# Kernel optimization log

Measured on AMD Instinct MI355X. Metric: run time of the kernel, lower is better.

The kernel has to match this reference:

```python
import jax, jax.numpy as jnp
import numpy as np

N_NODES = 50000
N_EDGES = 800000
IN_CH, HID_CH, OUT_CH = 128, 128, 64


def setup_inputs() -> dict:
    key = jax.random.key(0)
    k1, k2, k3, k4, k5, k6 = jax.random.split(key, 6)
    x = jax.random.normal(k1, (N_NODES, IN_CH), dtype=jnp.float32)
    edge_index = jax.random.randint(k2, (2, N_EDGES), 0, N_NODES, dtype=jnp.int64)
    # nn.Linear params: W [out, in], b [out]
    W1 = jax.random.normal(k3, (HID_CH, IN_CH), dtype=jnp.float32) / np.sqrt(IN_CH)
    b1 = jax.random.normal(k4, (HID_CH,), dtype=jnp.float32) * 0.01
    W2 = jax.random.normal(k5, (OUT_CH, HID_CH), dtype=jnp.float32) / np.sqrt(HID_CH)
    b2 = jax.random.normal(k6, (OUT_CH,), dtype=jnp.float32) * 0.01
    return {"x": x, "edge_index": edge_index, "W1": W1, "b1": b1, "W2": W2, "b2": b2}


def _aggregate(x, edge_index):
    # Faithful to SimpleGNN.aggregate: deg from ROW counts, normalization gathered at DST (col).
    row, col = edge_index[0], edge_index[1]
    n = x.shape[0]
    deg = jnp.bincount(row, length=n).astype(x.dtype)
    deg_inv = jnp.where(deg > 0, 1.0 / deg, 0.0)
    # out[dst] += x[src] * deg_inv[dst]  ==  segment_sum(x[src] by dst) * deg_inv[dst]
    agg = jax.ops.segment_sum(x[row], col, num_segments=n)
    return agg * deg_inv[:, None]


def reference(x, edge_index, W1, b1, W2, b2):
    h = x @ W1.T + b1                 # [N, hidden]
    h = _aggregate(h, edge_index)     # degree-normalized scatter-add
    out = h @ W2.T + b2               # [N, out]
    return out
```

## Files before the change

kernel.cpp:

```cpp
#include <hip/hip_runtime.h>
#include <hip/hip_bf16.h>


#define IN_CH   128
#define OUT_CH  64
#define NCHUNK  128
#define LGCHUNK 7
#define NRANGE  8
#define RBINS   6272
#define MC_BLOCKS 33
#define YROWS   32

typedef unsigned short u16;
typedef unsigned int u32;

static __device__ inline float bfu32_lo(u32 u) { return __uint_as_float(u << 16); }
static __device__ inline float bfu32_hi(u32 u) { return __uint_as_float(u & 0xffff0000u); }
static __device__ inline u16 f2bf(float f) {
    __hip_bfloat16 h = __float2bfloat16(f);
    return *reinterpret_cast<u16*>(&h);
}

static __device__ inline int detect_stride_wave(const int* __restrict__ ei) {
    int lane = threadIdx.x & 63;
    int idx = (lane < 32) ? (2 * lane + 1) : 1;
    int v = ei[idx];
    unsigned long long m = __ballot((v != 0) && (lane < 32));
    return (m == 0ull) ? 2 : 1;
}

__global__ __launch_bounds__(256) void mk_prep(const float* __restrict__ W1,
                                               const float* __restrict__ b1,
                                               const float* __restrict__ W2,
                                               const int* __restrict__ ei,
                                               float* __restrict__ M,
                                               float* __restrict__ c,
                                               u16* __restrict__ row_slab,
                                               u16* __restrict__ col_slab,
                                               int n_edges, int n_nodes) {
    __shared__ u32 bins[RBINS];
    int b = blockIdx.x;
    int tid = threadIdx.x;
    if (b < MC_BLOCKS) {
        int t = b * 256 + tid;
        if (t < IN_CH * OUT_CH) {
            int o = t & (OUT_CH - 1);
            int i = t >> 6;
            float acc = 0.f;
            for (int h = 0; h < 128; ++h)
                acc += W1[h * 128 + i] * W2[o * 128 + h];
            M[i * OUT_CH + o] = acc;
        } else if (t < IN_CH * OUT_CH + OUT_CH) {
            int o = t - IN_CH * OUT_CH;
            float acc = 0.f;
            for (int h = 0; h < 128; ++h)
                acc += b1[h] * W2[o * 128 + h];
            c[o] = acc;
        }
        return;
    }
    int hb = b - MC_BLOCKS;
    int chunk = hb & (NCHUNK - 1);
    int range = hb >> LGCHUNK;

    int range_size = (n_nodes + NRANGE - 1) / NRANGE;
    int lo = range * range_size;
    int hi = lo + range_size; if (hi > n_nodes) hi = n_nodes;
    int nbins = hi - lo;
    if (nbins <= 0) return;

    int stride = detect_stride_wave(ei);
    for (int i = tid; i < nbins; i += 256) bins[i] = 0u;
    __syncthreads();

    size_t e0 = (size_t)chunk * n_edges / NCHUNK;
    size_t e1 = (size_t)(chunk + 1) * n_edges / NCHUNK;
    size_t cnt = e1 - e0;
    const int* rp = ei;
    const int* cp = ei + (size_t)n_edges * stride;

    size_t i = tid;
    int s[8], d[8];
    for (; i + 1792 < cnt; i += 2048) {
#pragma unroll
        for (int k = 0; k < 8; ++k) s[k] = rp[(e0 + i + 256 * k) * stride];
#pragma unroll
        for (int k = 0; k < 8; ++k) d[k] = cp[(e0 + i + 256 * k) * stride];
#pragma unroll
        for (int k = 0; k < 8; ++k) {
            if (s[k] >= lo && s[k] < hi) atomicAdd(&bins[s[k] - lo], 1u);
            if (d[k] >= lo && d[k] < hi && (unsigned)s[k] < (unsigned)n_nodes)
                atomicAdd(&bins[d[k] - lo], 0x10000u);
        }
    }
    for (; i < cnt; i += 256) {
        int ss = rp[(e0 + i) * stride];
        int dd = cp[(e0 + i) * stride];
        if (ss >= lo && ss < hi) atomicAdd(&bins[ss - lo], 1u);
        if (dd >= lo && dd < hi && (unsigned)ss < (unsigned)n_nodes)
            atomicAdd(&bins[dd - lo], 0x10000u);
    }
    __syncthreads();

    size_t base = (size_t)chunk * n_nodes + lo;
    for (int k = tid; k < nbins; k += 256) {
        u32 v = bins[k];
        row_slab[base + k] = (u16)(v & 0xFFFFu);
        col_slab[base + k] = (u16)(v >> 16);
    }
}

__global__ __launch_bounds__(256) void mk_y_choff(const float* __restrict__ x,
                                                  const float* __restrict__ M,
                                                  u16* __restrict__ y,
                                                  u16* __restrict__ row_slab,
                                                  u16* __restrict__ col_slab,
                                                  int* __restrict__ deg_row,
                                                  int* __restrict__ cnt_col,
                                                  int* __restrict__ cursor_part,
                                                  int* __restrict__ bsums,
                                                  int n_nodes, int y_blocks) {
    __shared__ float smem[IN_CH * OUT_CH + YROWS * (IN_CH + 4)];
    int b = blockIdx.x;
    int tid = threadIdx.x;

    if (b < y_blocks) {
        float* Ms = smem;
        float (*xs)[IN_CH + 4] = (float(*)[IN_CH + 4])(smem + IN_CH * OUT_CH);
        int tx = tid & 15;
        int ty = tid >> 4;
        int row0 = b * YROWS;

        const float4* Mv = (const float4*)M;
        float4* Msv = (float4*)Ms;
#pragma unroll
        for (int k = 0; k < 8; ++k) Msv[tid + 256 * k] = Mv[tid + 256 * k];

        for (int f = tid; f < YROWS * 32; f += 256) {
            int r = f >> 5, kq = f & 31;
            float4 v = make_float4(0.f, 0.f, 0.f, 0.f);
            if (row0 + r < n_nodes)
                v = *(const float4*)&x[(size_t)(row0 + r) * IN_CH + 4 * kq];
            *(float4*)&xs[r][4 * kq] = v;
        }
        __syncthreads();

        float4 acc0 = make_float4(0.f, 0.f, 0.f, 0.f);
        float4 acc1 = make_float4(0.f, 0.f, 0.f, 0.f);

        for (int k = 0; k < IN_CH; k += 4) {
            float4 xr0 = *(const float4*)&xs[ty][k];
            float4 xr1 = *(const float4*)&xs[ty + 16][k];
            float4 m0 = *(const float4*)&Ms[(k + 0) * OUT_CH + 4 * tx];
            float4 m1 = *(const float4*)&Ms[(k + 1) * OUT_CH + 4 * tx];
            float4 m2 = *(const float4*)&Ms[(k + 2) * OUT_CH + 4 * tx];
            float4 m3 = *(const float4*)&Ms[(k + 3) * OUT_CH + 4 * tx];
            acc0.x = fmaf(xr0.x, m0.x, acc0.x); acc0.y = fmaf(xr0.x, m0.y, acc0.y);
            acc0.z = fmaf(xr0.x, m0.z, acc0.z); acc0.w = fmaf(xr0.x, m0.w, acc0.w);
            acc0.x = fmaf(xr0.y, m1.x, acc0.x); acc0.y = fmaf(xr0.y, m1.y, acc0.y);
            acc0.z = fmaf(xr0.y, m1.z, acc0.z); acc0.w = fmaf(xr0.y, m1.w, acc0.w);
            acc0.x = fmaf(xr0.z, m2.x, acc0.x); acc0.y = fmaf(xr0.z, m2.y, acc0.y);
            acc0.z = fmaf(xr0.z, m2.z, acc0.z); acc0.w = fmaf(xr0.z, m2.w, acc0.w);
            acc0.x = fmaf(xr0.w, m3.x, acc0.x); acc0.y = fmaf(xr0.w, m3.y, acc0.y);
            acc0.z = fmaf(xr0.w, m3.z, acc0.z); acc0.w = fmaf(xr0.w, m3.w, acc0.w);
            acc1.x = fmaf(xr1.x, m0.x, acc1.x); acc1.y = fmaf(xr1.x, m0.y, acc1.y);
            acc1.z = fmaf(xr1.x, m0.z, acc1.z); acc1.w = fmaf(xr1.x, m0.w, acc1.w);
            acc1.x = fmaf(xr1.y, m1.x, acc1.x); acc1.y = fmaf(xr1.y, m1.y, acc1.y);
            acc1.z = fmaf(xr1.y, m1.z, acc1.z); acc1.w = fmaf(xr1.y, m1.w, acc1.w);
            acc1.x = fmaf(xr1.z, m2.x, acc1.x); acc1.y = fmaf(xr1.z, m2.y, acc1.y);
            acc1.z = fmaf(xr1.z, m2.z, acc1.z); acc1.w = fmaf(xr1.z, m2.w, acc1.w);
            acc1.x = fmaf(xr1.w, m3.x, acc1.x); acc1.y = fmaf(xr1.w, m3.y, acc1.y);
            acc1.z = fmaf(xr1.w, m3.z, acc1.z); acc1.w = fmaf(xr1.w, m3.w, acc1.w);
        }

        int r0 = row0 + ty;
        int r1 = row0 + ty + 16;
        if (r0 < n_nodes) {
            ushort4 s4;
            s4.x = f2bf(acc0.x); s4.y = f2bf(acc0.y);
            s4.z = f2bf(acc0.z); s4.w = f2bf(acc0.w);
            *(ushort4*)&y[(size_t)r0 * OUT_CH + 4 * tx] = s4;
        }
        if (r1 < n_nodes) {
            ushort4 s4;
            s4.x = f2bf(acc1.x); s4.y = f2bf(acc1.y);
            s4.z = f2bf(acc1.z); s4.w = f2bf(acc1.w);
            *(ushort4*)&y[(size_t)r1 * OUT_CH + 4 * tx] = s4;
        }
        return;
    }

    int* sm = (int*)smem;
    int t = tid;
    int n = (b - y_blocks) * 256 + t;
    int run = 0;
    if (n < n_nodes) {
        int sum = 0;
#pragma unroll 8
        for (int ch = 0; ch < NCHUNK; ++ch)
            sum += row_slab[(size_t)ch * n_nodes + n];
        deg_row[n] = sum;
#pragma unroll 8
        for (int ch = 0; ch < NCHUNK; ++ch) {
            int v = col_slab[(size_t)ch * n_nodes + n];
            col_slab[(size_t)ch * n_nodes + n] = (u16)run;
            run += v;
        }
        cnt_col[n] = run;
    }
    sm[t] = run;
    __syncthreads();
    for (int d = 1; d < 256; d <<= 1) {
        int add = (t >= d) ? sm[t - d] : 0;
        __syncthreads();
        sm[t] += add;
        __syncthreads();
    }
    if (n < n_nodes) cursor_part[n] = sm[t] - run;
    if (t == 255) bsums[b - y_blocks] = sm[t];
}

static __device__ void block_bscan(const int* __restrict__ bsums, int nb,
                                   int* __restrict__ bscan) {
    int t = threadIdx.x;
    int v = (t < nb) ? bsums[t] : 0;
    bscan[t] = v;
    __syncthreads();
    for (int d = 1; d < 256; d <<= 1) {
        int add = (t >= d) ? bscan[t - d] : 0;
        __syncthreads();
        bscan[t] += add;
        __syncthreads();
    }
    bscan[t] -= v;
    __syncthreads();
}

__global__ __launch_bounds__(256) void mk_place(const int* __restrict__ ei,
                                                const int* __restrict__ cursor_part,
                                                const int* __restrict__ bsums,
                                                const u16* __restrict__ col_slab,
                                                int* __restrict__ csr_src,
                                                int n_edges, int n_nodes, int nb) {
    __shared__ int rank[RBINS];
    __shared__ int bscan[256];
    block_bscan(bsums, nb, bscan);

    int b = blockIdx.x;
    int chunk = b & (NCHUNK - 1);
    int range = b >> LGCHUNK;

    int range_size = (n_nodes + NRANGE - 1) / NRANGE;
    int lo = range * range_size;
    int hi = lo + range_size; if (hi > n_nodes) hi = n_nodes;
    if (hi <= lo) return;

    int stride = detect_stride_wave(ei);
    for (int i = threadIdx.x; i < hi - lo; i += 256) rank[i] = 0;
    __syncthreads();

    size_t e0 = (size_t)chunk * n_edges / NCHUNK;
    size_t e1 = (size_t)(chunk + 1) * n_edges / NCHUNK;
    size_t cnt = e1 - e0;
    const int* rp = ei;
    const int* cp = ei + (size_t)n_edges * stride;
    size_t slab_base = (size_t)chunk * n_nodes;

    size_t i = threadIdx.x;
    int s[8], d[8], cpart[8], coff[8];
    for (; i + 1792 < cnt; i += 2048) {
#pragma unroll
        for (int k = 0; k < 8; ++k) s[k] = rp[(e0 + i + 256 * k) * stride];
#pragma unroll
        for (int k = 0; k < 8; ++k) d[k] = cp[(e0 + i + 256 * k) * stride];
#pragma unroll
        for (int k = 0; k < 8; ++k) {
            int dc = (d[k] >= lo && d[k] < hi) ? d[k] : lo;
            cpart[k] = cursor_part[dc];
            coff[k]  = (int)col_slab[slab_base + dc];
        }
#pragma unroll
        for (int k = 0; k < 8; ++k) {
            if (d[k] >= lo && d[k] < hi && (unsigned)s[k] < (unsigned)n_nodes) {
                int r = atomicAdd(&rank[d[k] - lo], 1);
                csr_src[cpart[k] + bscan[d[k] >> 8] + coff[k] + r] = s[k];
            }
        }
    }
    for (; i < cnt; i += 256) {
        int ss = rp[(e0 + i) * stride];
        int dd = cp[(e0 + i) * stride];
        if (dd >= lo && dd < hi && (unsigned)ss < (unsigned)n_nodes) {
            int r = atomicAdd(&rank[dd - lo], 1);
            csr_src[cursor_part[dd] + bscan[dd >> 8] + (int)col_slab[slab_base + dd] + r] = ss;
        }
    }
}

__global__ __launch_bounds__(256) void mk_agg_final(const int* __restrict__ cursor_part,
                                                    const int* __restrict__ bsums,
                                                    const int* __restrict__ cnt_col,
                                                    const int* __restrict__ csr_src,
                                                    const int* __restrict__ deg_row,
                                                    const uint2* __restrict__ yv,
                                                    const float* __restrict__ c,
                                                    const float* __restrict__ b2,
                                                    float* __restrict__ out,
                                                    int n_nodes, int nb) {
    __shared__ int bscan[256];
    block_bscan(bsums, nb, bscan);

    int wave = threadIdx.x >> 6;
    int lane = threadIdx.x & 63;
    int dsub = lane >> 4;
    int ch   = lane & 15;
    int d = blockIdx.x * 16 + wave * 4 + dsub;
    if (d >= n_nodes) return;

    int start = cursor_part[d] + bscan[d >> 8];
    int cnt = cnt_col[d];
    int end = start + cnt;
    int e1m = end - 1;
    float a0 = 0.f, a1 = 0.f, a2 = 0.f, a3 = 0.f;
    for (int j = start; j < end; j += 8) {
        int idx[8], srcs[8];
#pragma unroll
        for (int k = 0; k < 8; ++k) {
            int t = j + k;
            idx[k] = t > e1m ? e1m : t;
        }
#pragma unroll
        for (int k = 0; k < 8; ++k) srcs[k] = csr_src[idx[k]];
        uint2 u[8];
#pragma unroll
        for (int k = 0; k < 8; ++k) u[k] = yv[(size_t)srcs[k] * 16 + ch];
#pragma unroll
        for (int k = 1; k < 8; ++k)
            if (j + k >= end) { u[k].x = 0u; u[k].y = 0u; }
#pragma unroll
        for (int k = 0; k < 8; ++k) {
            a0 += bfu32_lo(u[k].x);
            a1 += bfu32_hi(u[k].x);
            a2 += bfu32_lo(u[k].y);
            a3 += bfu32_hi(u[k].y);
        }
    }
    int dr = deg_row[d];
    float di = (dr > 0) ? (1.0f / (float)dr) : 0.f;
    float fc = di * (float)cnt;
    float4 cv = ((const float4*)c)[ch];
    float4 bv = ((const float4*)b2)[ch];
    float4 o;
    o.x = di * a0 + fc * cv.x + bv.x;
    o.y = di * a1 + fc * cv.y + bv.y;
    o.z = di * a2 + fc * cv.z + bv.z;
    o.w = di * a3 + fc * cv.w + bv.w;
    ((float4*)(out + (size_t)d * OUT_CH))[ch] = o;
}

extern "C" void kernel_launch(void* const* d_in, const int* in_sizes, int n_in,
                              void* d_out, int out_size, void* d_ws, size_t ws_size,
                              hipStream_t stream) {
    const float* x  = (const float*)d_in[0];
    const int*   ei = (const int*)d_in[1];
    const float* W1 = (const float*)d_in[2];
    const float* b1 = (const float*)d_in[3];
    const float* W2 = (const float*)d_in[4];
    const float* b2 = (const float*)d_in[5];
    float* out = (float*)d_out;

    const int n_nodes = in_sizes[0] / IN_CH;
    const int n_edges = in_sizes[1] / 2;

    const size_t slab_bytes = (((size_t)NCHUNK * n_nodes * 2) + 127) & ~(size_t)127;
    const size_t csr_bytes  = ((size_t)n_edges * 4 + 127) & ~(size_t)127;

    char* ws = (char*)d_ws;
    float* M        = (float*)(ws);
    float* c        = (float*)(ws + 32768);
    int*   deg_row  = (int*)  (ws + 33152);
    int*   cnt_col  = (int*)  (ws + 233216);
    int*   cursor   = (int*)  (ws + 433280);
    int*   bsums    = (int*)  (ws + 633344);
    u16*   row_slab = (u16*)  (ws + 637440);
    u16*   col_slab = (u16*)  (ws + 637440 + slab_bytes);
    int*   csr_src  = (int*)  (ws + 637440 + 2 * slab_bytes);
    u16*   y        = (u16*)  (ws + 637440 + 2 * slab_bytes + csr_bytes);

    const int y_blocks = (n_nodes + YROWS - 1) / YROWS;
    const int nb = (n_nodes + 255) / 256;

    mk_prep<<<MC_BLOCKS + NCHUNK * NRANGE, 256, 0, stream>>>(
        W1, b1, W2, ei, M, c, row_slab, col_slab, n_edges, n_nodes);

    mk_y_choff<<<y_blocks + nb, 256, 0, stream>>>(
        x, M, y, row_slab, col_slab, deg_row, cnt_col, cursor, bsums,
        n_nodes, y_blocks);

    mk_place<<<NCHUNK * NRANGE, 256, 0, stream>>>(
        ei, cursor, bsums, col_slab, csr_src, n_edges, n_nodes, nb);

    mk_agg_final<<<(n_nodes + 15) / 16, 256, 0, stream>>>(
        cursor, bsums, cnt_col, csr_src, deg_row, (const uint2*)y, c, b2, out,
        n_nodes, nb);
}
```

Measured before the change: 165.9 us.

## Move y GEMM into place kernel and halve edge chunk count

The x·M projection blocks move out of the prefix-sum kernel and into the CSR placement kernel, so the scan kernel is small and the GEMM overlaps with the edge scatter. The edge histogram uses 64 chunks instead of 128, which halves the slab size and the per-node work in the scan. Blocks are reordered so range is the fast index, and the M-compute blocks are padded to 40. Fewer chunks means each histogram/place block handles more edges, so there is less parallelism in those phases.

After: 154.9 us. 1.07x faster.

```diff
diff --git a/kernel.cpp b/kernel.cpp
--- a/kernel.cpp
+++ b/kernel.cpp
@@ -4,12 +4,14 @@
 
 #define IN_CH   128
 #define OUT_CH  64
-#define NCHUNK  128
-#define LGCHUNK 7
+#define NCHUNK  64
 #define NRANGE  8
 #define RBINS   6272
 #define MC_BLOCKS 33
+#define MC_PAD  40
 #define YROWS   32
+#define PLACE_BLOCKS (NCHUNK * NRANGE)
+#define SMEM_FLOATS (IN_CH * OUT_CH + YROWS * (IN_CH + 4))
 
 typedef unsigned short u16;
 typedef unsigned int u32;
@@ -41,7 +43,7 @@
     __shared__ u32 bins[RBINS];
     int b = blockIdx.x;
     int tid = threadIdx.x;
-    if (b < MC_BLOCKS) {
+    if (b < MC_PAD) {
         int t = b * 256 + tid;
         if (t < IN_CH * OUT_CH) {
             int o = t & (OUT_CH - 1);
@@ -59,9 +61,9 @@
         }
         return;
     }
-    int hb = b - MC_BLOCKS;
-    int chunk = hb & (NCHUNK - 1);
-    int range = hb >> LGCHUNK;
+    int hb = b - MC_PAD;
+    int range = hb & (NRANGE - 1);
+    int chunk = hb >> 3;
 
     int range_size = (n_nodes + NRANGE - 1) / NRANGE;
     int lo = range * range_size;
@@ -110,89 +112,16 @@
     }
 }
 
-__global__ __launch_bounds__(256) void mk_y_choff(const float* __restrict__ x,
-                                                  const float* __restrict__ M,
-                                                  u16* __restrict__ y,
-                                                  u16* __restrict__ row_slab,
-                                                  u16* __restrict__ col_slab,
-                                                  int* __restrict__ deg_row,
-                                                  int* __restrict__ cnt_col,
-                                                  int* __restrict__ cursor_part,
-                                                  int* __restrict__ bsums,
-                                                  int n_nodes, int y_blocks) {
-    __shared__ float smem[IN_CH * OUT_CH + YROWS * (IN_CH + 4)];
-    int b = blockIdx.x;
-    int tid = threadIdx.x;
-
-    if (b < y_blocks) {
-        float* Ms = smem;
-        float (*xs)[IN_CH + 4] = (float(*)[IN_CH + 4])(smem + IN_CH * OUT_CH);
-        int tx = tid & 15;
-        int ty = tid >> 4;
-        int row0 = b * YROWS;
-
-        const float4* Mv = (const float4*)M;
-        float4* Msv = (float4*)Ms;
-#pragma unroll
-        for (int k = 0; k < 8; ++k) Msv[tid + 256 * k] = Mv[tid + 256 * k];
-
-        for (int f = tid; f < YROWS * 32; f += 256) {
-            int r = f >> 5, kq = f & 31;
-            float4 v = make_float4(0.f, 0.f, 0.f, 0.f);
-            if (row0 + r < n_nodes)
-                v = *(const float4*)&x[(size_t)(row0 + r) * IN_CH + 4 * kq];
-            *(float4*)&xs[r][4 * kq] = v;
-        }
-        __syncthreads();
-
-        float4 acc0 = make_float4(0.f, 0.f, 0.f, 0.f);
-        float4 acc1 = make_float4(0.f, 0.f, 0.f, 0.f);
-
-        for (int k = 0; k < IN_CH; k += 4) {
-            float4 xr0 = *(const float4*)&xs[ty][k];
-            float4 xr1 = *(const float4*)&xs[ty + 16][k];
-            float4 m0 = *(const float4*)&Ms[(k + 0) * OUT_CH + 4 * tx];
-            float4 m1 = *(const float4*)&Ms[(k + 1) * OUT_CH + 4 * tx];
-            float4 m2 = *(const float4*)&Ms[(k + 2) * OUT_CH + 4 * tx];
-            float4 m3 = *(const float4*)&Ms[(k + 3) * OUT_CH + 4 * tx];
-            acc0.x = fmaf(xr0.x, m0.x, acc0.x); acc0.y = fmaf(xr0.x, m0.y, acc0.y);
-            acc0.z = fmaf(xr0.x, m0.z, acc0.z); acc0.w = fmaf(xr0.x, m0.w, acc0.w);
-            acc0.x = fmaf(xr0.y, m1.x, acc0.x); acc0.y = fmaf(xr0.y, m1.y, acc0.y);
-            acc0.z = fmaf(xr0.y, m1.z, acc0.z); acc0.w = fmaf(xr0.y, m1.w, acc0.w);
-            acc0.x = fmaf(xr0.z, m2.x, acc0.x); acc0.y = fmaf(xr0.z, m2.y, acc0.y);
-            acc0.z = fmaf(xr0.z, m2.z, acc0.z); acc0.w = fmaf(xr0.z, m2.w, acc0.w);
-            acc0.x = fmaf(xr0.w, m3.x, acc0.x); acc0.y = fmaf(xr0.w, m3.y, acc0.y);
-            acc0.z = fmaf(xr0.w, m3.z, acc0.z); acc0.w = fmaf(xr0.w, m3.w, acc0.w);
-            acc1.x = fmaf(xr1.x, m0.x, acc1.x); acc1.y = fmaf(xr1.x, m0.y, acc1.y);
-            acc1.z = fmaf(xr1.x, m0.z, acc1.z); acc1.w = fmaf(xr1.x, m0.w, acc1.w);
-            acc1.x = fmaf(xr1.y, m1.x, acc1.x); acc1.y = fmaf(xr1.y, m1.y, acc1.y);
-            acc1.z = fmaf(xr1.y, m1.z, acc1.z); acc1.w = fmaf(xr1.y, m1.w, acc1.w);
-            acc1.x = fmaf(xr1.z, m2.x, acc1.x); acc1.y = fmaf(xr1.z, m2.y, acc1.y);
-            acc1.z = fmaf(xr1.z, m2.z, acc1.z); acc1.w = fmaf(xr1.z, m2.w, acc1.w);
-            acc1.x = fmaf(xr1.w, m3.x, acc1.x); acc1.y = fmaf(xr1.w, m3.y, acc1.y);
-            acc1.z = fmaf(xr1.w, m3.z, acc1.z); acc1.w = fmaf(xr1.w, m3.w, acc1.w);
-        }
-
-        int r0 = row0 + ty;
-        int r1 = row0 + ty + 16;
-        if (r0 < n_nodes) {
-            ushort4 s4;
-            s4.x = f2bf(acc0.x); s4.y = f2bf(acc0.y);
-            s4.z = f2bf(acc0.z); s4.w = f2bf(acc0.w);
-            *(ushort4*)&y[(size_t)r0 * OUT_CH + 4 * tx] = s4;
-        }
-        if (r1 < n_nodes) {
-            ushort4 s4;
-            s4.x = f2bf(acc1.x); s4.y = f2bf(acc1.y);
-            s4.z = f2bf(acc1.z); s4.w = f2bf(acc1.w);
-            *(ushort4*)&y[(size_t)r1 * OUT_CH + 4 * tx] = s4;
-        }
-        return;
-    }
-
-    int* sm = (int*)smem;
-    int t = tid;
-    int n = (b - y_blocks) * 256 + t;
+__global__ __launch_bounds__(256) void mk_choff(u16* __restrict__ row_slab,
+                                                u16* __restrict__ col_slab,
+                                                int* __restrict__ deg_row,
+                                                int* __restrict__ cnt_col,
+                                                int* __restrict__ cursor_part,
+                                                int* __restrict__ bsums,
+                                                int n_nodes) {
+    __shared__ int sm[256];
+    int t = threadIdx.x;
+    int n = blockIdx.x * 256 + t;
     int run = 0;
     if (n < n_nodes) {
         int sum = 0;
@@ -217,7 +146,7 @@
         __syncthreads();
     }
     if (n < n_nodes) cursor_part[n] = sm[t] - run;
-    if (t == 255) bsums[b - y_blocks] = sm[t];
+    if (t == 255) bsums[blockIdx.x] = sm[t];
 }
 
 static __device__ void block_bscan(const int* __restrict__ bsums, int nb,
@@ -236,64 +165,137 @@
     __syncthreads();
 }
 
-__global__ __launch_bounds__(256) void mk_place(const int* __restrict__ ei,
-                                                const int* __restrict__ cursor_part,
-                                                const int* __restrict__ bsums,
-                                                const u16* __restrict__ col_slab,
-                                                int* __restrict__ csr_src,
-                                                int n_edges, int n_nodes, int nb) {
-    __shared__ int rank[RBINS];
-    __shared__ int bscan[256];
-    block_bscan(bsums, nb, bscan);
-
+__global__ __launch_bounds__(256) void mk_place_y(const int* __restrict__ ei,
+                                                  const int* __restrict__ cursor_part,
+                                                  const int* __restrict__ bsums,
+                                                  const u16* __restrict__ col_slab,
+                                                  int* __restrict__ csr_src,
+                                                  const float* __restrict__ x,
+                                                  const float* __restrict__ M,
+                                                  u16* __restrict__ y,
+                                                  int n_edges, int n_nodes, int nb) {
+    __shared__ float smem[SMEM_FLOATS];
     int b = blockIdx.x;
-    int chunk = b & (NCHUNK - 1);
-    int range = b >> LGCHUNK;
-
-    int range_size = (n_nodes + NRANGE - 1) / NRANGE;
-    int lo = range * range_size;
-    int hi = lo + range_size; if (hi > n_nodes) hi = n_nodes;
-    if (hi <= lo) return;
-
-    int stride = detect_stride_wave(ei);
-    for (int i = threadIdx.x; i < hi - lo; i += 256) rank[i] = 0;
-    __syncthreads();
-
-    size_t e0 = (size_t)chunk * n_edges / NCHUNK;
-    size_t e1 = (size_t)(chunk + 1) * n_edges / NCHUNK;
-    size_t cnt = e1 - e0;
-    const int* rp = ei;
-    const int* cp = ei + (size_t)n_edges * stride;
-    size_t slab_base = (size_t)chunk * n_nodes;
-
-    size_t i = threadIdx.x;
-    int s[8], d[8], cpart[8], coff[8];
-    for (; i + 1792 < cnt; i += 2048) {
-#pragma unroll
-        for (int k = 0; k < 8; ++k) s[k] = rp[(e0 + i + 256 * k) * stride];
-#pragma unroll
-        for (int k = 0; k < 8; ++k) d[k] = cp[(e0 + i + 256 * k) * stride];
-#pragma unroll
-        for (int k = 0; k < 8; ++k) {
-            int dc = (d[k] >= lo && d[k] < hi) ? d[k] : lo;
-            cpart[k] = cursor_part[dc];
-            coff[k]  = (int)col_slab[slab_base + dc];
-        }
-#pragma unroll
-        for (int k = 0; k < 8; ++k) {
-            if (d[k] >= lo && d[k] < hi && (unsigned)s[k] < (unsigned)n_nodes) {
-                int r = atomicAdd(&rank[d[k] - lo], 1);
-                csr_src[cpart[k] + bscan[d[k] >> 8] + coff[k] + r] = s[k];
+    int tid = threadIdx.x;
+
+    if (b < PLACE_BLOCKS) {
+        int* rank = (int*)smem;
+        int* bscan = (int*)smem + RBINS;
+        block_bscan(bsums, nb, bscan);
+
+        int range = b & (NRANGE - 1);
+        int chunk = b >> 3;
+        int range_size = (n_nodes + NRANGE - 1) / NRANGE;
+        int lo = range * range_size;
+        int hi = lo + range_size; if (hi > n_nodes) hi = n_nodes;
+        if (hi <= lo) return;
+
+        int stride = detect_stride_wave(ei);
+        for (int i = tid; i < hi - lo; i += 256) rank[i] = 0;
+        __syncthreads();
+
+        size_t e0 = (size_t)chunk * n_edges / NCHUNK;
+        size_t e1 = (size_t)(chunk + 1) * n_edges / NCHUNK;
+        size_t cnt = e1 - e0;
+        const int* rp = ei;
+        const int* cp = ei + (size_t)n_edges * stride;
+        size_t slab_base = (size_t)chunk * n_nodes;
+
+        size_t i = tid;
+        int s[8], d[8], cpart[8], coff[8];
+        for (; i + 1792 < cnt; i += 2048) {
+#pragma unroll
+            for (int k = 0; k < 8; ++k) s[k] = rp[(e0 + i + 256 * k) * stride];
+#pragma unroll
+            for (int k = 0; k < 8; ++k) d[k] = cp[(e0 + i + 256 * k) * stride];
+#pragma unroll
+            for (int k = 0; k < 8; ++k) {
+                int dc = (d[k] >= lo && d[k] < hi) ? d[k] : lo;
+                cpart[k] = cursor_part[dc];
+                coff[k]  = (int)col_slab[slab_base + dc];
             }
-        }
-    }
-    for (; i < cnt; i += 256) {
-        int ss = rp[(e0 + i) * stride];
-        int dd = cp[(e0 + i) * stride];
-        if (dd >= lo && dd < hi && (unsigned)ss < (unsigned)n_nodes) {
-            int r = atomicAdd(&rank[dd - lo], 1);
-            csr_src[cursor_part[dd] + bscan[dd >> 8] + (int)col_slab[slab_base + dd] + r] = ss;
-        }
+#pragma unroll
+            for (int k = 0; k < 8; ++k) {
+                if (d[k] >= lo && d[k] < hi && (unsigned)s[k] < (unsigned)n_nodes) {
+                    int r = atomicAdd(&rank[d[k] - lo], 1);
+                    csr_src[cpart[k] + bscan[d[k] >> 8] + coff[k] + r] = s[k];
+                }
+            }
+        }
+        for (; i < cnt; i += 256) {
+            int ss = rp[(e0 + i) * stride];
+            int dd = cp[(e0 + i) * stride];
+            if (dd >= lo && dd < hi && (unsigned)ss < (unsigned)n_nodes) {
+                int r = atomicAdd(&rank[dd - lo], 1);
+                csr_src[cursor_part[dd] + bscan[dd >> 8] + (int)col_slab[slab_base + dd] + r] = ss;
+            }
+        }
+        return;
+    }
+
+    int t = b - PLACE_BLOCKS;
+    float* Ms = smem;
+    float (*xs)[IN_CH + 4] = (float(*)[IN_CH + 4])(smem + IN_CH * OUT_CH);
+    int tx = tid & 15;
+    int ty = tid >> 4;
+    int row0 = t * YROWS;
+    if (row0 >= n_nodes) return;
+
+    const float4* Mv = (const float4*)M;
+    float4* Msv = (float4*)Ms;
+#pragma unroll
+    for (int k = 0; k < 8; ++k) Msv[tid + 256 * k] = Mv[tid + 256 * k];
+
+    for (int f = tid; f < YROWS * 32; f += 256) {
+        int r = f >> 5, kq = f & 31;
+        float4 v = make_float4(0.f, 0.f, 0.f, 0.f);
+        if (row0 + r < n_nodes)
+            v = *(const float4*)&x[(size_t)(row0 + r) * IN_CH + 4 * kq];
+        *(float4*)&xs[r][4 * kq] = v;
+    }
+    __syncthreads();
+
+    float4 acc0 = make_float4(0.f, 0.f, 0.f, 0.f);
+    float4 acc1 = make_float4(0.f, 0.f, 0.f, 0.f);
+
+    for (int k = 0; k < IN_CH; k += 4) {
+        float4 xr0 = *(const float4*)&xs[ty][k];
+        float4 xr1 = *(const float4*)&xs[ty + 16][k];
+        float4 m0 = *(const float4*)&Ms[(k + 0) * OUT_CH + 4 * tx];
+        float4 m1 = *(const float4*)&Ms[(k + 1) * OUT_CH + 4 * tx];
+        float4 m2 = *(const float4*)&Ms[(k + 2) * OUT_CH + 4 * tx];
+        float4 m3 = *(const float4*)&Ms[(k + 3) * OUT_CH + 4 * tx];
+        acc0.x = fmaf(xr0.x, m0.x, acc0.x); acc0.y = fmaf(xr0.x, m0.y, acc0.y);
+        acc0.z = fmaf(xr0.x, m0.z, acc0.z); acc0.w = fmaf(xr0.x, m0.w, acc0.w);
+        acc0.x = fmaf(xr0.y, m1.x, acc0.x); acc0.y = fmaf(xr0.y, m1.y, acc0.y);
+        acc0.z = fmaf(xr0.y, m1.z, acc0.z); acc0.w = fmaf(xr0.y, m1.w, acc0.w);
+        acc0.x = fmaf(xr0.z, m2.x, acc0.x); acc0.y = fmaf(xr0.z, m2.y, acc0.y);
+        acc0.z = fmaf(xr0.z, m2.z, acc0.z); acc0.w = fmaf(xr0.z, m2.w, acc0.w);
+        acc0.x = fmaf(xr0.w, m3.x, acc0.x); acc0.y = fmaf(xr0.w, m3.y, acc0.y);
+        acc0.z = fmaf(xr0.w, m3.z, acc0.z); acc0.w = fmaf(xr0.w, m3.w, acc0.w);
+        acc1.x = fmaf(xr1.x, m0.x, acc1.x); acc1.y = fmaf(xr1.x, m0.y, acc1.y);
+        acc1.z = fmaf(xr1.x, m0.z, acc1.z); acc1.w = fmaf(xr1.x, m0.w, acc1.w);
+        acc1.x = fmaf(xr1.y, m1.x, acc1.x); acc1.y = fmaf(xr1.y, m1.y, acc1.y);
+        acc1.z = fmaf(xr1.y, m1.z, acc1.z); acc1.w = fmaf(xr1.y, m1.w, acc1.w);
+        acc1.x = fmaf(xr1.z, m2.x, acc1.x); acc1.y = fmaf(xr1.z, m2.y, acc1.y);
+        acc1.z = fmaf(xr1.z, m2.z, acc1.z); acc1.w = fmaf(xr1.z, m2.w, acc1.w);
+        acc1.x = fmaf(xr1.w, m3.x, acc1.x); acc1.y = fmaf(xr1.w, m3.y, acc1.y);
+        acc1.z = fmaf(xr1.w, m3.z, acc1.z); acc1.w = fmaf(xr1.w, m3.w, acc1.w);
+    }
+
+    int r0 = row0 + ty;
+    int r1 = row0 + ty + 16;
+    if (r0 < n_nodes) {
+        ushort4 s4;
+        s4.x = f2bf(acc0.x); s4.y = f2bf(acc0.y);
+        s4.z = f2bf(acc0.z); s4.w = f2bf(acc0.w);
+        *(ushort4*)&y[(size_t)r0 * OUT_CH + 4 * tx] = s4;
+    }
+    if (r1 < n_nodes) {
+        ushort4 s4;
+        s4.x = f2bf(acc1.x); s4.y = f2bf(acc1.y);
+        s4.z = f2bf(acc1.z); s4.w = f2bf(acc1.w);
+        *(ushort4*)&y[(size_t)r1 * OUT_CH + 4 * tx] = s4;
     }
 }
 
@@ -390,15 +392,14 @@
     const int y_blocks = (n_nodes + YROWS - 1) / YROWS;
     const int nb = (n_nodes + 255) / 256;
 
-    mk_prep<<<MC_BLOCKS + NCHUNK * NRANGE, 256, 0, stream>>>(
+    mk_prep<<<MC_PAD + NCHUNK * NRANGE, 256, 0, stream>>>(
         W1, b1, W2, ei, M, c, row_slab, col_slab, n_edges, n_nodes);
 
-    mk_y_choff<<<y_blocks + nb, 256, 0, stream>>>(
-        x, M, y, row_slab, col_slab, deg_row, cnt_col, cursor, bsums,
-        n_nodes, y_blocks);
-
-    mk_place<<<NCHUNK * NRANGE, 256, 0, stream>>>(
-        ei, cursor, bsums, col_slab, csr_src, n_edges, n_nodes, nb);
+    mk_choff<<<nb, 256, 0, stream>>>(row_slab, col_slab, deg_row, cnt_col,
+                                     cursor, bsums, n_nodes);
+
+    mk_place_y<<<PLACE_BLOCKS + y_blocks, 256, 0, stream>>>(
+        ei, cursor, bsums, col_slab, csr_src, x, M, y, n_edges, n_nodes, nb);
 
     mk_agg_final<<<(n_nodes + 15) / 16, 256, 0, stream>>>(
         cursor, bsums, cnt_col, csr_src, deg_row, (const uint2*)y, c, b2, out,
```
